# Kernel tuning notes

Measured on AMD Instinct MI355X. Metric: run time of the kernel, lower is better.

## Reference

```python
import jax, jax.numpy as jnp
import numpy as np

ALPHA, BETA, LAMDA = 0.4, 2.0, 2.0
N_VIEWS, BATCH, DIM = 12, 4096, 128


def setup_inputs() -> dict:
    key = jax.random.key(0)
    k1, k2, k3, k4 = jax.random.split(key, 4)
    return {
        "SV_A": jax.random.normal(k1, (N_VIEWS, BATCH, DIM), dtype=jnp.float32),
        "SV_N": jax.random.normal(k2, (N_VIEWS, BATCH, DIM), dtype=jnp.float32),
        "MV_A": jax.random.normal(k3, (BATCH, DIM), dtype=jnp.float32),
        "MV_N": jax.random.normal(k4, (BATCH, DIM), dtype=jnp.float32),
    }


def reference(SV_A, SV_N, MV_A, MV_N):
    # expanded pairwise SQUARED distances across views, per batch element
    diff = SV_A[:, None, :, :] - SV_N[None, :, :, :]      # [nA, nN, B, D]
    d = jnp.sum(diff * diff, axis=-1)                     # [nA, nN, B]
    nA, nN, B = d.shape

    # hard-negative (confuser) mining: globally closest cross-object view pair per sample
    idx = jnp.argmin(d.reshape(nA * nN, B), axis=0)       # [B]
    conf_A = idx // nN
    conf_N = idx % nN
    b = jnp.arange(B)
    f_conf_A = SV_A[conf_A, b, :]                         # [B, D]
    f_conf_N = SV_N[conf_N, b, :]                         # [B, D]

    # inter-class distance between MV embeddings (euclidean, matches torch.cdist)
    mv_inter = jnp.sqrt(jnp.sum((MV_A - MV_N) ** 2, axis=-1))   # [B]
    # inter-class distance between confuser embeddings (squared, matches min of d)
    mc_inter = jnp.min(d, axis=(0, 1))                           # [B]
    # intra-class distances MV <-> confuser (euclidean)
    a_clstr = jnp.sqrt(jnp.sum((MV_A - f_conf_A) ** 2, axis=-1))  # [B]
    c_intra = jnp.sqrt(jnp.sum((MV_N - f_conf_N) ** 2, axis=-1))  # [B]

    loss_m_cluster = jax.nn.relu(a_clstr - ALPHA)
    loss_c_cluster = jax.nn.relu(c_intra - ALPHA)
    loss_mc_inter = jax.nn.relu(BETA - mc_inter)
    loss_mv_inter = jax.nn.relu(BETA - mv_inter)

    losses = LAMDA * (loss_mc_inter + loss_mv_inter) + loss_m_cluster + loss_c_cluster

    info_quads = [
        jnp.count_nonzero(losses),
        jnp.mean(jnp.sqrt(mc_inter)),
        0.5 * (jnp.mean(jnp.sqrt(a_clstr)) + jnp.mean(jnp.sqrt(c_intra))),
        jnp.min(jnp.sqrt(mc_inter)),
    ]
    avg_loss = jnp.mean(losses)
    return avg_loss, info_quads
```

## Files before the change

kernel.cpp:

```cpp
#include <hip/hip_runtime.h>
#include <math.h>

#define NV 12
#define BATCH 4096
#define DIM 128
#define ALPHA_C 0.4f
#define BETA_C 2.0f
#define LAMDA_C 2.0f
#define LDSPAD 132
#define BPB 4

__global__ __launch_bounds__(256) void perb_kernel(
    const float* __restrict__ SV_A, const float* __restrict__ SV_N,
    const float* __restrict__ MV_A, const float* __restrict__ MV_N,
    float4* __restrict__ perb)
{
    const int wave = threadIdx.x >> 6;
    const int lane = threadIdx.x & 63;
    const int b    = blockIdx.x * BPB + wave;

    __shared__ float As[BPB][NV][LDSPAD];
    __shared__ float Ns[BPB][NV][LDSPAD];
    __shared__ float normsA[BPB][NV];
    __shared__ float normsN[BPB][NV];

    const size_t mvoff = (size_t)b * DIM + lane;
    const float ma0 = MV_A[mvoff];
    const float ma1 = MV_A[mvoff + 64];
    const float mn0 = MV_N[mvoff];
    const float mn1 = MV_N[mvoff + 64];

    {
        const int half = lane >> 5;
        const int c    = (lane & 31) * 4;
        #pragma unroll
        for (int r = 0; r < NV / 2; ++r) {
            const int i = 2 * r + half;
            const size_t off = ((size_t)(i * BATCH + b)) * DIM + c;
            *(float4*)&As[wave][i][c] = *(const float4*)(SV_A + off);
            *(float4*)&Ns[wave][i][c] = *(const float4*)(SV_N + off);
        }
    }

    if (lane < 2 * NV) {
        const int arr = lane >= NV;
        const int row = arr ? (lane - NV) : lane;
        const float* p = arr ? Ns[wave][row] : As[wave][row];
        float nrm = 0.f;
        #pragma unroll
        for (int k = 0; k < DIM; k += 4) {
            const float4 v = *(const float4*)(p + k);
            nrm += v.x * v.x + v.y * v.y + v.z * v.z + v.w * v.w;
        }
        if (arr) normsN[wave][row] = nrm;
        else     normsA[wave][row] = nrm;
    }

    float best_d = 3.4e38f;
    int   best_p = 1 << 20;
    if (lane < 36) {
        const int i2 = lane / 6;
        const int j2 = lane % 6;
        const float* a0p = As[wave][2 * i2];
        const float* a1p = As[wave][2 * i2 + 1];
        const float* n0p = Ns[wave][2 * j2];
        const float* n1p = Ns[wave][2 * j2 + 1];
        float s00 = 0.f, s01 = 0.f, s10 = 0.f, s11 = 0.f;
        #pragma unroll
        for (int k = 0; k < DIM; k += 4) {
            const float4 a0 = *(const float4*)(a0p + k);
            const float4 a1 = *(const float4*)(a1p + k);
            const float4 n0 = *(const float4*)(n0p + k);
            const float4 n1 = *(const float4*)(n1p + k);
            s00 += a0.x * n0.x + a0.y * n0.y + a0.z * n0.z + a0.w * n0.w;
            s01 += a0.x * n1.x + a0.y * n1.y + a0.z * n1.z + a0.w * n1.w;
            s10 += a1.x * n0.x + a1.y * n0.y + a1.z * n0.z + a1.w * n0.w;
            s11 += a1.x * n1.x + a1.y * n1.y + a1.z * n1.z + a1.w * n1.w;
        }
        const float na0 = normsA[wave][2 * i2];
        const float na1 = normsA[wave][2 * i2 + 1];
        const float nn0 = normsN[wave][2 * j2];
        const float nn1 = normsN[wave][2 * j2 + 1];
        const float d00 = na0 + nn0 - 2.f * s00;
        const float d01 = na0 + nn1 - 2.f * s01;
        const float d10 = na1 + nn0 - 2.f * s10;
        const float d11 = na1 + nn1 - 2.f * s11;
        const int p00 = (2 * i2) * NV + 2 * j2;
        best_d = d00; best_p = p00;
        if (d01 < best_d) { best_d = d01; best_p = p00 + 1; }
        if (d10 < best_d) { best_d = d10; best_p = p00 + NV; }
        if (d11 < best_d) { best_d = d11; best_p = p00 + NV + 1; }
    }

    #pragma unroll
    for (int off = 32; off > 0; off >>= 1) {
        const float od = __shfl_down(best_d, off, 64);
        const int   op = __shfl_down(best_p, off, 64);
        if (od < best_d || (od == best_d && op < best_p)) { best_d = od; best_p = op; }
    }
    best_d = __shfl(best_d, 0, 64);
    best_p = __shfl(best_p, 0, 64);

    const int istar = best_p / NV;
    const int jstar = best_p % NV;

    float sa, sc, sm;
    {
        const float fa0 = As[wave][istar][lane];
        const float fa1 = As[wave][istar][lane + 64];
        const float fn0 = Ns[wave][jstar][lane];
        const float fn1 = Ns[wave][jstar][lane + 64];
        float d1;
        d1 = ma0 - fa0; sa  = d1 * d1;
        d1 = ma1 - fa1; sa += d1 * d1;
        d1 = mn0 - fn0; sc  = d1 * d1;
        d1 = mn1 - fn1; sc += d1 * d1;
        d1 = ma0 - mn0; sm  = d1 * d1;
        d1 = ma1 - mn1; sm += d1 * d1;
    }
    #pragma unroll
    for (int off = 32; off > 0; off >>= 1) {
        sa += __shfl_down(sa, off, 64);
        sc += __shfl_down(sc, off, 64);
        sm += __shfl_down(sm, off, 64);
    }

    if (lane == 0) {
        const float mc    = fmaxf(best_d, 0.f);
        const float a_cl  = sqrtf(sa);
        const float c_in  = sqrtf(sc);
        const float mv_in = sqrtf(sm);
        const float loss  = LAMDA_C * (fmaxf(BETA_C - mc, 0.f) + fmaxf(BETA_C - mv_in, 0.f))
                          + fmaxf(a_cl - ALPHA_C, 0.f) + fmaxf(c_in - ALPHA_C, 0.f);
        float4 o;
        o.x = loss;
        o.y = (loss != 0.f) ? 1.f : 0.f;
        o.z = sqrtf(mc);
        o.w = 0.5f * (sqrtf(a_cl) + sqrtf(c_in));
        perb[b] = o;
    }
}

__global__ __launch_bounds__(1024) void final_kernel(
    const float4* __restrict__ perb, float* __restrict__ out)
{
    const int t = threadIdx.x;
    float sl = 0.f, sn = 0.f, ss = 0.f, sh = 0.f, mnv = 3.4e38f;
    #pragma unroll
    for (int u = 0; u < BATCH / 1024; ++u) {
        const float4 v = perb[t + u * 1024];
        sl += v.x; sn += v.y; ss += v.z; sh += v.w;
        mnv = fminf(mnv, v.z);
    }
    #pragma unroll
    for (int off = 32; off > 0; off >>= 1) {
        sl += __shfl_down(sl, off, 64);
        sn += __shfl_down(sn, off, 64);
        ss += __shfl_down(ss, off, 64);
        sh += __shfl_down(sh, off, 64);
        mnv = fminf(mnv, __shfl_down(mnv, off, 64));
    }
    __shared__ float r[16][5];
    const int w = t >> 6;
    if ((t & 63) == 0) {
        r[w][0] = sl; r[w][1] = sn; r[w][2] = ss; r[w][3] = sh; r[w][4] = mnv;
    }
    __syncthreads();
    if (t == 0) {
        #pragma unroll
        for (int i = 1; i < 16; ++i) {
            sl += r[i][0]; sn += r[i][1]; ss += r[i][2]; sh += r[i][3];
            mnv = fminf(mnv, r[i][4]);
        }
        const float inv = 1.0f / (float)BATCH;
        out[0] = sl * inv;
        out[1] = sn;
        out[2] = ss * inv;
        out[3] = sh * inv;
        out[4] = mnv;
    }
}

extern "C" void kernel_launch(void* const* d_in, const int* in_sizes, int n_in,
                              void* d_out, int out_size, void* d_ws, size_t ws_size,
                              hipStream_t stream) {
    const float* SV_A = (const float*)d_in[0];
    const float* SV_N = (const float*)d_in[1];
    const float* MV_A = (const float*)d_in[2];
    const float* MV_N = (const float*)d_in[3];
    float* out = (float*)d_out;
    float4* perb = (float4*)d_ws;

    perb_kernel<<<BATCH / BPB, 256, 0, stream>>>(SV_A, SV_N, MV_A, MV_N, perb);
    final_kernel<<<1, 1024, 0, stream>>>(perb, out);
}
```

Baseline: 99.53 us.

## Register-tile pairwise dots with K-split and fuse final reduction via atomics

```diff
diff --git a/kernel.cpp b/kernel.cpp
--- a/kernel.cpp
+++ b/kernel.cpp
@@ -10,19 +10,24 @@
 #define LDSPAD 132
 #define BPB 4
 
+__device__ __forceinline__ float dot4(const float4 a, const float4 b) {
+    return a.x * b.x + a.y * b.y + a.z * b.z + a.w * b.w;
+}
+
 __global__ __launch_bounds__(256) void perb_kernel(
     const float* __restrict__ SV_A, const float* __restrict__ SV_N,
     const float* __restrict__ MV_A, const float* __restrict__ MV_N,
-    float4* __restrict__ perb)
+    float* __restrict__ out)
 {
     const int wave = threadIdx.x >> 6;
     const int lane = threadIdx.x & 63;
     const int b    = blockIdx.x * BPB + wave;
 
-    __shared__ float As[BPB][NV][LDSPAD];
-    __shared__ float Ns[BPB][NV][LDSPAD];
-    __shared__ float normsA[BPB][NV];
-    __shared__ float normsN[BPB][NV];
+    __shared__ __align__(16) float As[BPB][NV][LDSPAD];
+    __shared__ __align__(16) float Ns[BPB][NV][LDSPAD];
+    __shared__ __align__(16) float normsA[BPB][NV];
+    __shared__ __align__(16) float normsN[BPB][NV];
+    __shared__ float comm[BPB][5];
 
     const size_t mvoff = (size_t)b * DIM + lane;
     const float ma0 = MV_A[mvoff];
@@ -32,68 +37,90 @@
 
     {
         const int half = lane >> 5;
-        const int c    = (lane & 31) * 4;
+        const int c4   = (lane & 31) * 4;
         #pragma unroll
         for (int r = 0; r < NV / 2; ++r) {
             const int i = 2 * r + half;
-            const size_t off = ((size_t)(i * BATCH + b)) * DIM + c;
-            *(float4*)&As[wave][i][c] = *(const float4*)(SV_A + off);
-            *(float4*)&Ns[wave][i][c] = *(const float4*)(SV_N + off);
-        }
-    }
-
-    if (lane < 2 * NV) {
-        const int arr = lane >= NV;
-        const int row = arr ? (lane - NV) : lane;
-        const float* p = arr ? Ns[wave][row] : As[wave][row];
+            const size_t off = ((size_t)(i * BATCH + b)) * DIM + c4;
+            *(float4*)&As[wave][i][c4] = *(const float4*)(SV_A + off);
+            *(float4*)&Ns[wave][i][c4] = *(const float4*)(SV_N + off);
+        }
+    }
+
+    {
         float nrm = 0.f;
-        #pragma unroll
-        for (int k = 0; k < DIM; k += 4) {
-            const float4 v = *(const float4*)(p + k);
-            nrm += v.x * v.x + v.y * v.y + v.z * v.z + v.w * v.w;
-        }
-        if (arr) normsN[wave][row] = nrm;
-        else     normsA[wave][row] = nrm;
-    }
+        if (lane < 48) {
+            const int rr  = lane % 24;
+            const int h   = lane / 24;
+            const int arr = rr >= NV;
+            const int row = arr ? rr - NV : rr;
+            const float* p = (arr ? &Ns[wave][row][0] : &As[wave][row][0]) + h * 64;
+            #pragma unroll
+            for (int k = 0; k < 64; k += 4) {
+                const float4 v = *(const float4*)(p + k);
+                nrm += dot4(v, v);
+            }
+        }
+        nrm += __shfl_down(nrm, 24, 64);
+        if (lane < 2 * NV) {
+            const int arr = lane >= NV;
+            const int row = arr ? lane - NV : lane;
+            if (arr) normsN[wave][row] = nrm;
+            else     normsA[wave][row] = nrm;
+        }
+    }
+
+    const int tile = lane % 9;
+    const int q    = lane / 9;
+    const int ti   = tile / 3;
+    const int tj   = tile % 3;
+    float dots[4][4] = {{0.f, 0.f, 0.f, 0.f}, {0.f, 0.f, 0.f, 0.f},
+                        {0.f, 0.f, 0.f, 0.f}, {0.f, 0.f, 0.f, 0.f}};
+    if (lane < 36) {
+        const float* Abase = &As[wave][4 * ti][0] + q * 32;
+        const float* Nbase = &Ns[wave][4 * tj][0] + q * 32;
+        #pragma unroll
+        for (int s = 0; s < 8; ++s) {
+            float4 av[4], nv[4];
+            #pragma unroll
+            for (int r = 0; r < 4; ++r) av[r] = *(const float4*)(Abase + r * LDSPAD + s * 4);
+            #pragma unroll
+            for (int c = 0; c < 4; ++c) nv[c] = *(const float4*)(Nbase + c * LDSPAD + s * 4);
+            #pragma unroll
+            for (int r = 0; r < 4; ++r)
+                #pragma unroll
+                for (int c = 0; c < 4; ++c)
+                    dots[r][c] += dot4(av[r], nv[c]);
+        }
+    }
+    #pragma unroll
+    for (int r = 0; r < 4; ++r)
+        #pragma unroll
+        for (int c = 0; c < 4; ++c) {
+            float v = dots[r][c];
+            v += __shfl_down(v, 18, 64);
+            v += __shfl_down(v, 9, 64);
+            dots[r][c] = v;
+        }
 
     float best_d = 3.4e38f;
     int   best_p = 1 << 20;
-    if (lane < 36) {
-        const int i2 = lane / 6;
-        const int j2 = lane % 6;
-        const float* a0p = As[wave][2 * i2];
-        const float* a1p = As[wave][2 * i2 + 1];
-        const float* n0p = Ns[wave][2 * j2];
-        const float* n1p = Ns[wave][2 * j2 + 1];
-        float s00 = 0.f, s01 = 0.f, s10 = 0.f, s11 = 0.f;
-        #pragma unroll
-        for (int k = 0; k < DIM; k += 4) {
-            const float4 a0 = *(const float4*)(a0p + k);
-            const float4 a1 = *(const float4*)(a1p + k);
-            const float4 n0 = *(const float4*)(n0p + k);
-            const float4 n1 = *(const float4*)(n1p + k);
-            s00 += a0.x * n0.x + a0.y * n0.y + a0.z * n0.z + a0.w * n0.w;
-            s01 += a0.x * n1.x + a0.y * n1.y + a0.z * n1.z + a0.w * n1.w;
-            s10 += a1.x * n0.x + a1.y * n0.y + a1.z * n0.z + a1.w * n0.w;
-            s11 += a1.x * n1.x + a1.y * n1.y + a1.z * n1.z + a1.w * n1.w;
-        }
-        const float na0 = normsA[wave][2 * i2];
-        const float na1 = normsA[wave][2 * i2 + 1];
-        const float nn0 = normsN[wave][2 * j2];
-        const float nn1 = normsN[wave][2 * j2 + 1];
-        const float d00 = na0 + nn0 - 2.f * s00;
-        const float d01 = na0 + nn1 - 2.f * s01;
-        const float d10 = na1 + nn0 - 2.f * s10;
-        const float d11 = na1 + nn1 - 2.f * s11;
-        const int p00 = (2 * i2) * NV + 2 * j2;
-        best_d = d00; best_p = p00;
-        if (d01 < best_d) { best_d = d01; best_p = p00 + 1; }
-        if (d10 < best_d) { best_d = d10; best_p = p00 + NV; }
-        if (d11 < best_d) { best_d = d11; best_p = p00 + NV + 1; }
-    }
-
+    if (lane < 9) {
+        const float4 na4 = *(const float4*)&normsA[wave][4 * ti];
+        const float4 nn4 = *(const float4*)&normsN[wave][4 * tj];
+        const float na[4] = {na4.x, na4.y, na4.z, na4.w};
+        const float nn[4] = {nn4.x, nn4.y, nn4.z, nn4.w};
+        #pragma unroll
+        for (int r = 0; r < 4; ++r)
+            #pragma unroll
+            for (int c = 0; c < 4; ++c) {
+                const float d = na[r] + nn[c] - 2.f * dots[r][c];
+                const int   p = (4 * ti + r) * NV + (4 * tj + c);
+                if (d < best_d) { best_d = d; best_p = p; }
+            }
+    }
     #pragma unroll
-    for (int off = 32; off > 0; off >>= 1) {
+    for (int off = 8; off > 0; off >>= 1) {
         const float od = __shfl_down(best_d, off, 64);
         const int   op = __shfl_down(best_p, off, 64);
         if (od < best_d || (od == best_d && op < best_p)) { best_d = od; best_p = op; }
@@ -132,52 +159,28 @@
         const float mv_in = sqrtf(sm);
         const float loss  = LAMDA_C * (fmaxf(BETA_C - mc, 0.f) + fmaxf(BETA_C - mv_in, 0.f))
                           + fmaxf(a_cl - ALPHA_C, 0.f) + fmaxf(c_in - ALPHA_C, 0.f);
-        float4 o;
-        o.x = loss;
-        o.y = (loss != 0.f) ? 1.f : 0.f;
-        o.z = sqrtf(mc);
-        o.w = 0.5f * (sqrtf(a_cl) + sqrtf(c_in));
-        perb[b] = o;
-    }
-}
-
-__global__ __launch_bounds__(1024) void final_kernel(
-    const float4* __restrict__ perb, float* __restrict__ out)
-{
-    const int t = threadIdx.x;
-    float sl = 0.f, sn = 0.f, ss = 0.f, sh = 0.f, mnv = 3.4e38f;
-    #pragma unroll
-    for (int u = 0; u < BATCH / 1024; ++u) {
-        const float4 v = perb[t + u * 1024];
-        sl += v.x; sn += v.y; ss += v.z; sh += v.w;
-        mnv = fminf(mnv, v.z);
-    }
-    #pragma unroll
-    for (int off = 32; off > 0; off >>= 1) {
-        sl += __shfl_down(sl, off, 64);
-        sn += __shfl_down(sn, off, 64);
-        ss += __shfl_down(ss, off, 64);
-        sh += __shfl_down(sh, off, 64);
-        mnv = fminf(mnv, __shfl_down(mnv, off, 64));
-    }
-    __shared__ float r[16][5];
-    const int w = t >> 6;
-    if ((t & 63) == 0) {
-        r[w][0] = sl; r[w][1] = sn; r[w][2] = ss; r[w][3] = sh; r[w][4] = mnv;
+        const float z = sqrtf(mc);
+        comm[wave][0] = loss;
+        comm[wave][1] = (loss != 0.f) ? 1.f : 0.f;
+        comm[wave][2] = z;
+        comm[wave][3] = 0.5f * (sqrtf(a_cl) + sqrtf(c_in));
+        comm[wave][4] = z;
     }
     __syncthreads();
-    if (t == 0) {
-        #pragma unroll
-        for (int i = 1; i < 16; ++i) {
-            sl += r[i][0]; sn += r[i][1]; ss += r[i][2]; sh += r[i][3];
-            mnv = fminf(mnv, r[i][4]);
+
+    if (threadIdx.x == 0) {
+        float sl = 0.f, sn = 0.f, ss = 0.f, sh = 0.f, mn = 3.4e38f;
+        #pragma unroll
+        for (int w = 0; w < BPB; ++w) {
+            sl += comm[w][0]; sn += comm[w][1]; ss += comm[w][2]; sh += comm[w][3];
+            mn = fminf(mn, comm[w][4]);
         }
         const float inv = 1.0f / (float)BATCH;
-        out[0] = sl * inv;
-        out[1] = sn;
-        out[2] = ss * inv;
-        out[3] = sh * inv;
-        out[4] = mnv;
+        atomicAdd(&out[0], sl * inv);
+        atomicAdd(&out[1], sn);
+        atomicAdd(&out[2], ss * inv);
+        atomicAdd(&out[3], sh * inv);
+        atomicMin((unsigned int*)&out[4], __float_as_uint(mn));
     }
 }
 
@@ -189,8 +192,9 @@
     const float* MV_A = (const float*)d_in[2];
     const float* MV_N = (const float*)d_in[3];
     float* out = (float*)d_out;
-    float4* perb = (float4*)d_ws;
-
-    perb_kernel<<<BATCH / BPB, 256, 0, stream>>>(SV_A, SV_N, MV_A, MV_N, perb);
-    final_kernel<<<1, 1024, 0, stream>>>(perb, out);
+
+    hipMemsetAsync(out, 0, (size_t)out_size * sizeof(float), stream);
+    hipMemsetAsync((char*)out + 4 * sizeof(float), 0xFF, sizeof(float), stream);
+
+    perb_kernel<<<BATCH / BPB, 256, 0, stream>>>(SV_A, SV_N, MV_A, MV_N, out);
 }
```

After: 157.5 us. 58.2% more time.

## Compute view Gram matrix with split-bf16 MFMA instead of scalar FP32 dot products

Applied to the files above, without the earlier changes.

```diff
diff --git a/kernel.cpp b/kernel.cpp
--- a/kernel.cpp
+++ b/kernel.cpp
@@ -7,8 +7,20 @@
 #define ALPHA_C 0.4f
 #define BETA_C 2.0f
 #define LAMDA_C 2.0f
-#define LDSPAD 132
 #define BPB 4
+#define HPAD 136
+#define GPAD 26
+
+typedef short short8 __attribute__((ext_vector_type(8)));
+typedef float f32x16 __attribute__((ext_vector_type(16)));
+
+__device__ __forceinline__ unsigned short f2bf(float f) {
+    unsigned int u = __float_as_uint(f);
+    return (unsigned short)((u + 0x7fffu + ((u >> 16) & 1u)) >> 16);
+}
+__device__ __forceinline__ float bf2f(unsigned short s) {
+    return __uint_as_float(((unsigned int)s) << 16);
+}
 
 __global__ __launch_bounds__(256) void perb_kernel(
     const float* __restrict__ SV_A, const float* __restrict__ SV_N,
@@ -19,10 +31,9 @@
     const int lane = threadIdx.x & 63;
     const int b    = blockIdx.x * BPB + wave;
 
-    __shared__ float As[BPB][NV][LDSPAD];
-    __shared__ float Ns[BPB][NV][LDSPAD];
-    __shared__ float normsA[BPB][NV];
-    __shared__ float normsN[BPB][NV];
+    __shared__ __align__(16) unsigned short Hi[BPB][24][HPAD];
+    __shared__ __align__(16) unsigned short Lo[BPB][24][HPAD];
+    __shared__ __align__(16) float G[BPB][24][GPAD];
 
     const size_t mvoff = (size_t)b * DIM + lane;
     const float ma0 = MV_A[mvoff];
@@ -32,28 +43,56 @@
 
     {
         const int half = lane >> 5;
-        const int c    = (lane & 31) * 4;
+        const int c4   = (lane & 31) * 4;
         #pragma unroll
-        for (int r = 0; r < NV / 2; ++r) {
-            const int i = 2 * r + half;
-            const size_t off = ((size_t)(i * BATCH + b)) * DIM + c;
-            *(float4*)&As[wave][i][c] = *(const float4*)(SV_A + off);
-            *(float4*)&Ns[wave][i][c] = *(const float4*)(SV_N + off);
-        }
-    }
-
-    if (lane < 2 * NV) {
-        const int arr = lane >= NV;
-        const int row = arr ? (lane - NV) : lane;
-        const float* p = arr ? Ns[wave][row] : As[wave][row];
-        float nrm = 0.f;
+        for (int rr = 0; rr < NV / 2; ++rr) {
+            const int i = 2 * rr + half;
+            const size_t off = ((size_t)(i * BATCH + b)) * DIM + c4;
+            #pragma unroll
+            for (int arr = 0; arr < 2; ++arr) {
+                const float4 v = *(const float4*)((arr ? SV_N : SV_A) + off);
+                const unsigned short h0 = f2bf(v.x), h1 = f2bf(v.y);
+                const unsigned short h2 = f2bf(v.z), h3 = f2bf(v.w);
+                const unsigned short l0 = f2bf(v.x - bf2f(h0));
+                const unsigned short l1 = f2bf(v.y - bf2f(h1));
+                const unsigned short l2 = f2bf(v.z - bf2f(h2));
+                const unsigned short l3 = f2bf(v.w - bf2f(h3));
+                const int row = arr * NV + i;
+                uint2 hw, lw;
+                hw.x = (unsigned int)h0 | ((unsigned int)h1 << 16);
+                hw.y = (unsigned int)h2 | ((unsigned int)h3 << 16);
+                lw.x = (unsigned int)l0 | ((unsigned int)l1 << 16);
+                lw.y = (unsigned int)l2 | ((unsigned int)l3 << 16);
+                *(uint2*)&Hi[wave][row][c4] = hw;
+                *(uint2*)&Lo[wave][row][c4] = lw;
+            }
+        }
+    }
+
+    {
+        int r = lane & 31;
+        if (r >= 24) r = 0;
+        const int h = lane >> 5;
+        const unsigned short* hbase = &Hi[wave][r][h * 8];
+        const unsigned short* lbase = &Lo[wave][r][h * 8];
+        f32x16 acc = {0.f, 0.f, 0.f, 0.f, 0.f, 0.f, 0.f, 0.f,
+                      0.f, 0.f, 0.f, 0.f, 0.f, 0.f, 0.f, 0.f};
         #pragma unroll
-        for (int k = 0; k < DIM; k += 4) {
-            const float4 v = *(const float4*)(p + k);
-            nrm += v.x * v.x + v.y * v.y + v.z * v.z + v.w * v.w;
-        }
-        if (arr) normsN[wave][row] = nrm;
-        else     normsA[wave][row] = nrm;
+        for (int kb = 0; kb < 8; ++kb) {
+            const short8 hv = *(const short8*)(hbase + kb * 16);
+            const short8 lv = *(const short8*)(lbase + kb * 16);
+            acc = __builtin_amdgcn_mfma_f32_32x32x16_bf16(hv, hv, acc, 0, 0, 0);
+            acc = __builtin_amdgcn_mfma_f32_32x32x16_bf16(hv, lv, acc, 0, 0, 0);
+            acc = __builtin_amdgcn_mfma_f32_32x32x16_bf16(lv, hv, acc, 0, 0, 0);
+        }
+        const int col = lane & 31;
+        if (col < 24) {
+            #pragma unroll
+            for (int rg = 0; rg < 12; ++rg) {
+                const int row = (rg & 3) + 8 * (rg >> 2) + 4 * h;
+                G[wave][row][col] = acc[rg];
+            }
+        }
     }
 
     float best_d = 3.4e38f;
@@ -61,37 +100,24 @@
     if (lane < 36) {
         const int i2 = lane / 6;
         const int j2 = lane % 6;
-        const float* a0p = As[wave][2 * i2];
-        const float* a1p = As[wave][2 * i2 + 1];
-        const float* n0p = Ns[wave][2 * j2];
-        const float* n1p = Ns[wave][2 * j2 + 1];
-        float s00 = 0.f, s01 = 0.f, s10 = 0.f, s11 = 0.f;
-        #pragma unroll
-        for (int k = 0; k < DIM; k += 4) {
-            const float4 a0 = *(const float4*)(a0p + k);
-            const float4 a1 = *(const float4*)(a1p + k);
-            const float4 n0 = *(const float4*)(n0p + k);
-            const float4 n1 = *(const float4*)(n1p + k);
-            s00 += a0.x * n0.x + a0.y * n0.y + a0.z * n0.z + a0.w * n0.w;
-            s01 += a0.x * n1.x + a0.y * n1.y + a0.z * n1.z + a0.w * n1.w;
-            s10 += a1.x * n0.x + a1.y * n0.y + a1.z * n0.z + a1.w * n0.w;
-            s11 += a1.x * n1.x + a1.y * n1.y + a1.z * n1.z + a1.w * n1.w;
-        }
-        const float na0 = normsA[wave][2 * i2];
-        const float na1 = normsA[wave][2 * i2 + 1];
-        const float nn0 = normsN[wave][2 * j2];
-        const float nn1 = normsN[wave][2 * j2 + 1];
-        const float d00 = na0 + nn0 - 2.f * s00;
-        const float d01 = na0 + nn1 - 2.f * s01;
-        const float d10 = na1 + nn0 - 2.f * s10;
-        const float d11 = na1 + nn1 - 2.f * s11;
-        const int p00 = (2 * i2) * NV + 2 * j2;
+        const int ia0 = 2 * i2, ia1 = 2 * i2 + 1;
+        const int jn0 = 12 + 2 * j2, jn1 = jn0 + 1;
+        const float2 g0 = *(const float2*)&G[wave][ia0][jn0];
+        const float2 g1 = *(const float2*)&G[wave][ia1][jn0];
+        const float na0 = G[wave][ia0][ia0];
+        const float na1 = G[wave][ia1][ia1];
+        const float nn0 = G[wave][jn0][jn0];
+        const float nn1 = G[wave][jn1][jn1];
+        const float d00 = na0 + nn0 - 2.f * g0.x;
+        const float d01 = na0 + nn1 - 2.f * g0.y;
+        const float d10 = na1 + nn0 - 2.f * g1.x;
+        const float d11 = na1 + nn1 - 2.f * g1.y;
+        const int p00 = ia0 * NV + 2 * j2;
         best_d = d00; best_p = p00;
         if (d01 < best_d) { best_d = d01; best_p = p00 + 1; }
         if (d10 < best_d) { best_d = d10; best_p = p00 + NV; }
         if (d11 < best_d) { best_d = d11; best_p = p00 + NV + 1; }
     }
-
     #pragma unroll
     for (int off = 32; off > 0; off >>= 1) {
         const float od = __shfl_down(best_d, off, 64);
@@ -106,10 +132,12 @@
 
     float sa, sc, sm;
     {
-        const float fa0 = As[wave][istar][lane];
-        const float fa1 = As[wave][istar][lane + 64];
-        const float fn0 = Ns[wave][jstar][lane];
-        const float fn1 = Ns[wave][jstar][lane + 64];
+        const size_t offA = ((size_t)(istar * BATCH + b)) * DIM + lane;
+        const size_t offN = ((size_t)(jstar * BATCH + b)) * DIM + lane;
+        const float fa0 = SV_A[offA];
+        const float fa1 = SV_A[offA + 64];
+        const float fn0 = SV_N[offN];
+        const float fn1 = SV_N[offN + 64];
         float d1;
         d1 = ma0 - fa0; sa  = d1 * d1;
         d1 = ma1 - fa1; sa += d1 * d1;
```

New measurement: 97.65 us. Within noise of the previous version (-1.9%).
